# Kernel tuning notes

Hardware: AMD Instinct MI355X
Metric: run time of the kernel (lower is better)

## Reference

```python
import jax, jax.numpy as jnp
import numpy as np

B, N, C = 8, 8192, 91
H = W = 800
SCORE_THRESH = 0.05
NMS_THRESH = 0.5
DET_PER_IMG = 100
BBOX_XFORM_CLIP = float(np.log(1000.0 / 16.0))
WX, WY, WW, WH = 10.0, 10.0, 5.0, 5.0  # bbox_reg_weights


def setup_inputs() -> dict:
    key = jax.random.key(0)
    k1, k2, k3, k4 = jax.random.split(key, 4)
    # realistic xyxy proposals inside the image
    cxcy = jax.random.uniform(k1, (B, N, 2)) * jnp.array([W, H], jnp.float32)
    wh = 8.0 + jax.random.uniform(k2, (B, N, 2)) * 192.0
    x1y1 = jnp.clip(cxcy - 0.5 * wh, 0.0, None)
    x2y2 = jnp.minimum(cxcy + 0.5 * wh, jnp.array([W, H], jnp.float32))
    proposals = jnp.concatenate([x1y1, x2y2], axis=-1)
    class_logits = jax.random.normal(k3, (B, N, C)) * 2.0
    box_regression = jax.random.normal(k4, (B, N, C * 4)) * 0.1
    return {"class_logits": class_logits, "box_regression": box_regression,
            "proposals": proposals}


def _iou_one_many(box, boxes):
    # box [4], boxes [M,4] -> IoU [M] (box_ops.box_iou row)
    lt = jnp.maximum(box[:2], boxes[:, :2])
    rb = jnp.minimum(box[2:], boxes[:, 2:])
    wh = jnp.clip(rb - lt, 0.0, None)
    inter = wh[:, 0] * wh[:, 1]
    a1 = (box[2] - box[0]) * (box[3] - box[1])
    a2 = (boxes[:, 2] - boxes[:, 0]) * (boxes[:, 3] - boxes[:, 1])
    return inter / (a1 + a2 - inter + 1e-9)


def _postprocess_one(logits, codes, props):
    # logits [N,C], codes [N,C,4], props [N,4]
    # --- BoxCoder.decode ---
    widths = props[:, 2] - props[:, 0]
    heights = props[:, 3] - props[:, 1]
    ctr_x = props[:, 0] + 0.5 * widths
    ctr_y = props[:, 1] + 0.5 * heights
    dx = codes[..., 0] / WX
    dy = codes[..., 1] / WY
    dw = jnp.minimum(codes[..., 2] / WW, BBOX_XFORM_CLIP)
    dh = jnp.minimum(codes[..., 3] / WH, BBOX_XFORM_CLIP)
    pcx = dx * widths[:, None] + ctr_x[:, None]
    pcy = dy * heights[:, None] + ctr_y[:, None]
    pw = jnp.exp(dw) * widths[:, None]
    ph = jnp.exp(dh) * heights[:, None]
    boxes = jnp.stack([pcx - 0.5 * pw, pcy - 0.5 * ph,
                       pcx + 0.5 * pw, pcy + 0.5 * ph], axis=-1)  # [N,C,4]
    scores = jax.nn.softmax(logits, axis=-1)
    # --- clip_boxes_to_image ---
    boxes = jnp.stack([jnp.clip(boxes[..., 0], 0.0, float(W)),
                       jnp.clip(boxes[..., 1], 0.0, float(H)),
                       jnp.clip(boxes[..., 2], 0.0, float(W)),
                       jnp.clip(boxes[..., 3], 0.0, float(H))], axis=-1)
    # --- drop background class 0, flatten candidates ---
    boxes = boxes[:, 1:].reshape(-1, 4)          # [M,4], M = N*(C-1)
    scores = scores[:, 1:].reshape(-1)           # [M]
    labels = jnp.tile(jnp.arange(1, C, dtype=jnp.int32), N)  # [M]
    # --- score threshold + remove_small_boxes(min_size=1.0), as masks ---
    ws = boxes[:, 2] - boxes[:, 0]
    hs = boxes[:, 3] - boxes[:, 1]
    valid = (scores > SCORE_THRESH) & (ws >= 1.0) & (hs >= 1.0)
    live = jnp.where(valid, scores, -1.0)
    # --- batched_nms via per-class coordinate offset ---
    off = labels.astype(boxes.dtype) * (float(max(H, W)) + 1.0)
    nboxes = boxes + off[:, None]

    def step(live, _):
        i = jnp.argmax(live)
        s = live[i]
        ious = _iou_one_many(nboxes[i], nboxes)
        live = jnp.where(ious > NMS_THRESH, -1.0, live)
        live = live.at[i].set(-1.0)
        return live, (boxes[i], s, labels[i])

    _, (db, ds, dl) = jax.lax.scan(step, live, None, length=DET_PER_IMG)
    ok = ds > 0.0  # sentinel -1 marks exhausted/invalid slots
    db = jnp.where(ok[:, None], db, 0.0)
    ds = jnp.where(ok, ds, 0.0)
    dl = jnp.where(ok, dl, 0)
    return db, ds, dl, ok


def reference(class_logits, box_regression, proposals):
    codes = box_regression.reshape(B, N, C, 4)
    boxes, scores, labels, valid = jax.vmap(_postprocess_one)(
        class_logits, codes, proposals)
    return boxes, scores, labels, valid
```

## Files before the change

kernel.cpp:

```cpp
#include <hip/hip_runtime.h>

#define BIMG 8
#define NPROP 8192
#define NCLS 91
#define WIMG 800.0f
#define HIMG 800.0f
#define SCORE_T 0.05f
#define NMS_T 0.5f
#define NDET 100
#define CLIPV 4.135166556742356f
#define CNT_STRIDE 16
#define NSURV 100
#define MAXK 512
#define MCACHE 32

__device__ __forceinline__ unsigned long long packkey(float s, int idx) {
    return ((unsigned long long)__float_as_uint(s) << 32) |
           (unsigned long long)(0xFFFFFFFFu - (unsigned int)idx);
}

__global__ void zero_kernel(int* p, int n) {
    int i = blockIdx.x * blockDim.x + threadIdx.x;
    if (i < n) p[i] = 0;
}

__global__ __launch_bounds__(256)
void decode_kernel(const float* __restrict__ logits,
                   const float* __restrict__ creg,
                   const float* __restrict__ props,
                   float* __restrict__ CX1, float* __restrict__ CY1,
                   float* __restrict__ CX2, float* __restrict__ CY2,
                   float* __restrict__ CS, int* __restrict__ CIDX,
                   int* __restrict__ cnt, int capC)
{
    const int wave = blockIdx.x * 4 + (threadIdx.x >> 6);
    const int lane = threadIdx.x & 63;
    const int row = wave;
    const int b = row >> 13;
    const int n = row & (NPROP - 1);

    const float* lrow = logits + (size_t)row * NCLS;
    const float l0 = lrow[lane];
    const float l1 = (lane + 64 < NCLS) ? lrow[lane + 64] : -3.4e38f;

    float m = fmaxf(l0, l1);
    for (int mm = 32; mm > 0; mm >>= 1) m = fmaxf(m, __shfl_xor(m, mm));

    const float e0 = expf(l0 - m);
    const float e1 = (lane + 64 < NCLS) ? expf(l1 - m) : 0.0f;

    float s = e0 + e1;
    for (int mm = 32; mm > 0; mm >>= 1) s += __shfl_xor(s, mm);
    const float denom = __shfl(s, 0);

    const float* p = props + (size_t)row * 4;
    const float px1 = p[0], py1 = p[1], px2 = p[2], py2 = p[3];
    const float w = px2 - px1, h = py2 - py1;
    const float cx = px1 + 0.5f * w, cy = py1 + 0.5f * h;

    for (int half = 0; half < 2; ++half) {
        const int c = lane + half * 64;
        if (c < 1 || c >= NCLS) continue;
        const float score = (half ? e1 : e0) / denom;
        if (!(score > SCORE_T)) continue;

        const float* cd = creg + ((size_t)row * NCLS + c) * 4;
        const float dx = cd[0] / 10.0f;
        const float dy = cd[1] / 10.0f;
        const float dw = fminf(cd[2] / 5.0f, CLIPV);
        const float dh = fminf(cd[3] / 5.0f, CLIPV);
        const float pcx = dx * w + cx, pcy = dy * h + cy;
        const float pw = expf(dw) * w, ph = expf(dh) * h;
        float bx1 = pcx - 0.5f * pw, by1 = pcy - 0.5f * ph;
        float bx2 = pcx + 0.5f * pw, by2 = pcy + 0.5f * ph;
        bx1 = fminf(fmaxf(bx1, 0.0f), WIMG);
        by1 = fminf(fmaxf(by1, 0.0f), HIMG);
        bx2 = fminf(fmaxf(bx2, 0.0f), WIMG);
        by2 = fminf(fmaxf(by2, 0.0f), HIMG);
        if ((bx2 - bx1) >= 1.0f && (by2 - by1) >= 1.0f) {
            const int bc = b * NCLS + c;
            const int k = atomicAdd(&cnt[bc * CNT_STRIDE], 1);
            if (k < capC) {
                const size_t o = (size_t)bc * capC + k;
                CX1[o] = bx1; CY1[o] = by1; CX2[o] = bx2; CY2[o] = by2;
                CS[o] = score;
                CIDX[o] = n * (NCLS - 1) + (c - 1);
            }
        }
    }
}

__global__ __launch_bounds__(256)
void nms_class_kernel(const float* __restrict__ CX1, const float* __restrict__ CY1,
                      const float* __restrict__ CX2, const float* __restrict__ CY2,
                      const float* __restrict__ CS, const int* __restrict__ CIDX,
                      const int* __restrict__ cnt,
                      float* __restrict__ SX1, float* __restrict__ SY1,
                      float* __restrict__ SX2, float* __restrict__ SY2,
                      float* __restrict__ SS, int* __restrict__ SIDX,
                      int* __restrict__ scnt, int capC)
{
    const int bc = blockIdx.x;
    const int c = bc % NCLS;
    const int tid = threadIdx.x;
    const int lane = tid & 63;
    const int wv = tid >> 6;

    int K = 0;
    if (c != 0) {
        K = cnt[bc * CNT_STRIDE];
        if (K > capC) K = capC;
        if (K > MAXK) K = MAXK;
    }
    if (K == 0) { if (tid == 0) scnt[bc] = 0; return; }

    __shared__ float bx1[MAXK], by1[MAXK], bx2[MAXK], by2[MAXK], bs[MAXK];
    __shared__ int bidx[MAXK];
    __shared__ unsigned long long keys[MAXK];
    __shared__ unsigned long long mask[MAXK * 8];
    __shared__ int wseq[NSURV];
    __shared__ int nselsh;

    const size_t base = (size_t)bc * capC;
    for (int i = tid; i < K; i += 256) {
        const float v0 = CX1[base + i], v1 = CY1[base + i];
        const float v2 = CX2[base + i], v3 = CY2[base + i];
        const float sv = CS[base + i];
        const int ix = CIDX[base + i];
        bx1[i] = v0; by1[i] = v1; bx2[i] = v2; by2[i] = v3;
        bs[i] = sv; bidx[i] = ix;
        keys[i] = packkey(sv, ix);
    }
    __syncthreads();

    float* tf = (float*)mask;
    int*   ti = (int*)mask;
    for (int i = tid; i < K; i += 256) {
        const unsigned long long k = keys[i];
        int r = 0;
        for (int j = 0; j < K; ++j) r += (keys[j] > k) ? 1 : 0;
        tf[0 * MAXK + r] = bx1[i];
        tf[1 * MAXK + r] = by1[i];
        tf[2 * MAXK + r] = bx2[i];
        tf[3 * MAXK + r] = by2[i];
        tf[4 * MAXK + r] = bs[i];
        ti[5 * MAXK + r] = bidx[i];
    }
    __syncthreads();
    for (int i = tid; i < K; i += 256) {
        bx1[i] = tf[0 * MAXK + i]; by1[i] = tf[1 * MAXK + i];
        bx2[i] = tf[2 * MAXK + i]; by2[i] = tf[3 * MAXK + i];
        bs[i]  = tf[4 * MAXK + i]; bidx[i] = ti[5 * MAXK + i];
    }
    __syncthreads();

    const float off = (float)c * 801.0f;
    const int W = (K + 63) >> 6;
    for (int w = wv; w < W; w += 4) {
        const int j = (w << 6) + lane;
        const bool jv = (j < K);
        float jx1 = 0, jy1 = 0, jx2 = 0, jy2 = 0;
        if (jv) {
            jx1 = bx1[j] + off; jy1 = by1[j] + off;
            jx2 = bx2[j] + off; jy2 = by2[j] + off;
        }
        const float a2 = (jx2 - jx1) * (jy2 - jy1);
        for (int a = 0; a < K; ++a) {
            const float ax1 = bx1[a] + off, ay1 = by1[a] + off;
            const float ax2 = bx2[a] + off, ay2 = by2[a] + off;
            const float ta = (ax2 - ax1) * (ay2 - ay1);
            bool sup = false;
            if (jv) {
                const float ltx = fmaxf(ax1, jx1), lty = fmaxf(ay1, jy1);
                const float rbx = fminf(ax2, jx2), rby = fminf(ay2, jy2);
                const float iw = fmaxf(rbx - ltx, 0.0f);
                const float ih = fmaxf(rby - lty, 0.0f);
                const float inter = iw * ih;
                const float iou = inter / (ta + a2 - inter + 1e-9f);
                sup = iou > NMS_T;
            }
            const unsigned long long bal = __ballot(sup);
            if (lane == 0) mask[a * 8 + w] = bal;
        }
    }
    __syncthreads();

    if (wv == 0) {
        unsigned long long aw = 0ull;
        if (lane < 8) {
            const int lo = lane << 6;
            if (K > lo) {
                const int nb = K - lo;
                aw = (nb >= 64) ? ~0ull : ((1ull << nb) - 1ull);
            }
        }
        int nsel = 0;
        while (nsel < NSURV) {
            int pos = 0x7fffffff;
            if (aw) pos = (lane << 6) + __builtin_ctzll(aw);
            for (int mm = 32; mm > 0; mm >>= 1)
                pos = min(pos, __shfl_xor(pos, mm));
            if (pos == 0x7fffffff) break;
            if (lane == 0) wseq[nsel] = pos;
            if (lane < 8) aw &= ~mask[(size_t)pos * 8 + lane];
            ++nsel;
        }
        if (lane == 0) nselsh = nsel;
    }
    __syncthreads();

    const int nsel = nselsh;
    for (int t = tid; t < nsel; t += 256) {
        const int a = wseq[t];
        const int sb = bc * NSURV + t;
        SX1[sb] = bx1[a]; SY1[sb] = by1[a];
        SX2[sb] = bx2[a]; SY2[sb] = by2[a];
        SS[sb] = bs[a]; SIDX[sb] = bidx[a];
    }
    if (tid == 0) scnt[bc] = nsel;
}

__global__ __launch_bounds__(256)
void merge_kernel(const float* __restrict__ SX1, const float* __restrict__ SY1,
                  const float* __restrict__ SX2, const float* __restrict__ SY2,
                  const float* __restrict__ SS, const int* __restrict__ SIDX,
                  const int* __restrict__ scnt, float* __restrict__ out)
{
    const int b = blockIdx.x;
    const int tid = threadIdx.x;
    const int lane = tid & 63;
    const int wv = tid >> 6;

    __shared__ unsigned long long kc[NCLS * MCACHE];
    __shared__ int scs[NCLS];
    __shared__ int wseq[NDET];
    __shared__ int stepsh;

    for (int i = tid; i < NCLS; i += 256) scs[i] = scnt[b * NCLS + i];
    __syncthreads();
    for (int t = tid; t < NCLS * MCACHE; t += 256) {
        const int cc = t >> 5, h = t & (MCACHE - 1);
        unsigned long long k = 0ull;
        if (cc >= 1 && h < scs[cc]) {
            const int sb = (b * NCLS + cc) * NSURV + h;
            k = packkey(SS[sb], SIDX[sb]);
        }
        kc[t] = k;
    }
    __syncthreads();

    if (wv == 0) {
        const int c1 = 1 + lane;
        const int c2 = 65 + lane;
        const bool v2 = (c2 < NCLS);
        int h1 = 0, h2 = 0;
        const int s1 = scs[c1];
        const int s2 = v2 ? scs[c2] : 0;
        unsigned long long k1 = (s1 > 0) ? kc[c1 * MCACHE] : 0ull;
        unsigned long long k2 = (s2 > 0) ? kc[c2 * MCACHE] : 0ull;
        int step = 0;
        while (step < NDET) {
            unsigned long long mk = (k1 > k2) ? k1 : k2;
            for (int mm = 32; mm > 0; mm >>= 1) {
                const unsigned long long o = __shfl_xor(mk, mm);
                if (o > mk) mk = o;
            }
            if (mk == 0ull) break;
            if (k1 == mk) {
                wseq[step] = (c1 << 16) | h1;
                ++h1;
                k1 = (h1 < s1)
                     ? (h1 < MCACHE ? kc[c1 * MCACHE + h1]
                                    : packkey(SS[(b * NCLS + c1) * NSURV + h1],
                                              SIDX[(b * NCLS + c1) * NSURV + h1]))
                     : 0ull;
            } else if (k2 == mk) {
                wseq[step] = (c2 << 16) | h2;
                ++h2;
                k2 = (h2 < s2)
                     ? (h2 < MCACHE ? kc[c2 * MCACHE + h2]
                                    : packkey(SS[(b * NCLS + c2) * NSURV + h2],
                                              SIDX[(b * NCLS + c2) * NSURV + h2]))
                     : 0ull;
            }
            ++step;
        }
        if (lane == 0) stepsh = step;
    }
    __syncthreads();

    const int OB = 0, OS = BIMG * NDET * 4, OL = OS + BIMG * NDET,
              OV = OL + BIMG * NDET;
    const int step = stepsh;
    for (int t = tid; t < NDET; t += 256) {
        const int o = b * NDET + t;
        if (t < step) {
            const int cw = wseq[t] >> 16, h = wseq[t] & 0xFFFF;
            const int sb = (b * NCLS + cw) * NSURV + h;
            out[OB + o * 4 + 0] = SX1[sb]; out[OB + o * 4 + 1] = SY1[sb];
            out[OB + o * 4 + 2] = SX2[sb]; out[OB + o * 4 + 3] = SY2[sb];
            out[OS + o] = SS[sb];
            out[OL + o] = (float)cw;
            out[OV + o] = 1.0f;
        } else {
            out[OB + o * 4 + 0] = 0.0f; out[OB + o * 4 + 1] = 0.0f;
            out[OB + o * 4 + 2] = 0.0f; out[OB + o * 4 + 3] = 0.0f;
            out[OS + o] = 0.0f; out[OL + o] = 0.0f; out[OV + o] = 0.0f;
        }
    }
}

extern "C" void kernel_launch(void* const* d_in, const int* in_sizes, int n_in,
                              void* d_out, int out_size, void* d_ws, size_t ws_size,
                              hipStream_t stream) {
    const float* logits = (const float*)d_in[0];
    const float* creg   = (const float*)d_in[1];
    const float* props  = (const float*)d_in[2];
    float* out = (float*)d_out;

    const int nCnt = BIMG * NCLS * CNT_STRIDE;
    const int nZero = nCnt + BIMG * NCLS;
    int* cnt = (int*)d_ws;
    int* scnt = cnt + nCnt;

    const size_t survSlots = (size_t)BIMG * NCLS * NSURV;
    float* SX1 = (float*)((char*)d_ws + 49504);
    float* SY1 = SX1 + survSlots;
    float* SX2 = SY1 + survSlots;
    float* SY2 = SX2 + survSlots;
    float* SS  = SY2 + survSlots;
    int*   SIDX = (int*)(SS + survSlots);

    const size_t clBase = 49504 + survSlots * 6 * 4;
    long capC = 256;
    if (ws_size > clBase) {
        capC = (long)((ws_size - clBase) / ((size_t)BIMG * NCLS * 24));
        capC &= ~63L;
        if (capC < 256) capC = 256;
        if (capC > MAXK) capC = MAXK;
    }
    const size_t clSlots = (size_t)BIMG * NCLS * capC;
    float* CX1 = (float*)((char*)d_ws + clBase);
    float* CY1 = CX1 + clSlots;
    float* CX2 = CY1 + clSlots;
    float* CY2 = CX2 + clSlots;
    float* CS  = CY2 + clSlots;
    int*   CIDX = (int*)(CS + clSlots);

    zero_kernel<<<(nZero + 255) / 256, 256, 0, stream>>>(cnt, nZero);
    decode_kernel<<<BIMG * NPROP / 4, 256, 0, stream>>>(
        logits, creg, props, CX1, CY1, CX2, CY2, CS, CIDX, cnt, (int)capC);
    nms_class_kernel<<<BIMG * NCLS, 256, 0, stream>>>(
        CX1, CY1, CX2, CY2, CS, CIDX, cnt,
        SX1, SY1, SX2, SY2, SS, SIDX, scnt, (int)capC);
    merge_kernel<<<BIMG, 256, 0, stream>>>(
        SX1, SY1, SX2, SY2, SS, SIDX, scnt, out);
}
```

Measured before the change: 492.1 us.

## Pack candidates as float4 boxes plus 64-bit keys, triangular NMS mask, histogram-based top-k merge

Candidate and survivor storage moves from six structure-of-arrays buffers to a float4 box array plus a packed 64-bit score/index key, so loads and stores are vectorized. The IoU mask is now computed only for the upper triangle (j > a), and the greedy NMS selection scans eight words per lane instead of doing a cross-lane shuffle reduction. The serial wave-level k-way merge is replaced by a 1024-thread histogram over score bits, a prefix scan to find the threshold bucket, tie resolution, and rank-by-counting. The histogram bucketing assumes a score range and a MAXTIE cap of 256, which risks wrong results if many keys fall into the threshold bucket.

```diff
diff --git a/kernel.cpp b/kernel.cpp
--- a/kernel.cpp
+++ b/kernel.cpp
@@ -12,11 +12,12 @@
 #define CNT_STRIDE 16
 #define NSURV 100
 #define MAXK 512
-#define MCACHE 32
-
-__device__ __forceinline__ unsigned long long packkey(float s, int idx) {
+#define NBUCK 1024
+#define MAXTIE 256
+
+__device__ __forceinline__ unsigned long long packkey(float s, unsigned int idx) {
     return ((unsigned long long)__float_as_uint(s) << 32) |
-           (unsigned long long)(0xFFFFFFFFu - (unsigned int)idx);
+           (unsigned long long)(0xFFFFFFFFu - idx);
 }
 
 __global__ void zero_kernel(int* p, int n) {
@@ -28,9 +29,8 @@
 void decode_kernel(const float* __restrict__ logits,
                    const float* __restrict__ creg,
                    const float* __restrict__ props,
-                   float* __restrict__ CX1, float* __restrict__ CY1,
-                   float* __restrict__ CX2, float* __restrict__ CY2,
-                   float* __restrict__ CS, int* __restrict__ CIDX,
+                   float4* __restrict__ CBOX,
+                   unsigned long long* __restrict__ CKEY,
                    int* __restrict__ cnt, int capC)
 {
     const int wave = blockIdx.x * 4 + (threadIdx.x >> 6);
@@ -53,10 +53,9 @@
     for (int mm = 32; mm > 0; mm >>= 1) s += __shfl_xor(s, mm);
     const float denom = __shfl(s, 0);
 
-    const float* p = props + (size_t)row * 4;
-    const float px1 = p[0], py1 = p[1], px2 = p[2], py2 = p[3];
-    const float w = px2 - px1, h = py2 - py1;
-    const float cx = px1 + 0.5f * w, cy = py1 + 0.5f * h;
+    const float4 p4 = ((const float4*)props)[row];
+    const float w = p4.z - p4.x, h = p4.w - p4.y;
+    const float cx = p4.x + 0.5f * w, cy = p4.y + 0.5f * h;
 
     for (int half = 0; half < 2; ++half) {
         const int c = lane + half * 64;
@@ -64,11 +63,11 @@
         const float score = (half ? e1 : e0) / denom;
         if (!(score > SCORE_T)) continue;
 
-        const float* cd = creg + ((size_t)row * NCLS + c) * 4;
-        const float dx = cd[0] / 10.0f;
-        const float dy = cd[1] / 10.0f;
-        const float dw = fminf(cd[2] / 5.0f, CLIPV);
-        const float dh = fminf(cd[3] / 5.0f, CLIPV);
+        const float4 cd = ((const float4*)creg)[(size_t)row * NCLS + c];
+        const float dx = cd.x / 10.0f;
+        const float dy = cd.y / 10.0f;
+        const float dw = fminf(cd.z / 5.0f, CLIPV);
+        const float dh = fminf(cd.w / 5.0f, CLIPV);
         const float pcx = dx * w + cx, pcy = dy * h + cy;
         const float pw = expf(dw) * w, ph = expf(dh) * h;
         float bx1 = pcx - 0.5f * pw, by1 = pcy - 0.5f * ph;
@@ -82,22 +81,19 @@
             const int k = atomicAdd(&cnt[bc * CNT_STRIDE], 1);
             if (k < capC) {
                 const size_t o = (size_t)bc * capC + k;
-                CX1[o] = bx1; CY1[o] = by1; CX2[o] = bx2; CY2[o] = by2;
-                CS[o] = score;
-                CIDX[o] = n * (NCLS - 1) + (c - 1);
+                CBOX[o] = make_float4(bx1, by1, bx2, by2);
+                CKEY[o] = packkey(score, (unsigned int)(n * (NCLS - 1) + (c - 1)));
             }
         }
     }
 }
 
 __global__ __launch_bounds__(256)
-void nms_class_kernel(const float* __restrict__ CX1, const float* __restrict__ CY1,
-                      const float* __restrict__ CX2, const float* __restrict__ CY2,
-                      const float* __restrict__ CS, const int* __restrict__ CIDX,
+void nms_class_kernel(const float4* __restrict__ CBOX,
+                      const unsigned long long* __restrict__ CKEY,
                       const int* __restrict__ cnt,
-                      float* __restrict__ SX1, float* __restrict__ SY1,
-                      float* __restrict__ SX2, float* __restrict__ SY2,
-                      float* __restrict__ SS, int* __restrict__ SIDX,
+                      float4* __restrict__ SBOX,
+                      unsigned long long* __restrict__ SKEY,
                       int* __restrict__ scnt, int capC)
 {
     const int bc = blockIdx.x;
@@ -114,44 +110,31 @@
     }
     if (K == 0) { if (tid == 0) scnt[bc] = 0; return; }
 
-    __shared__ float bx1[MAXK], by1[MAXK], bx2[MAXK], by2[MAXK], bs[MAXK];
-    __shared__ int bidx[MAXK];
-    __shared__ unsigned long long keys[MAXK];
-    __shared__ unsigned long long mask[MAXK * 8];
+    __shared__ float4 sbox[MAXK];
+    __shared__ unsigned long long skey[MAXK];
+    __shared__ __align__(16) unsigned long long mask[MAXK * 8];
     __shared__ int wseq[NSURV];
     __shared__ int nselsh;
 
     const size_t base = (size_t)bc * capC;
     for (int i = tid; i < K; i += 256) {
-        const float v0 = CX1[base + i], v1 = CY1[base + i];
-        const float v2 = CX2[base + i], v3 = CY2[base + i];
-        const float sv = CS[base + i];
-        const int ix = CIDX[base + i];
-        bx1[i] = v0; by1[i] = v1; bx2[i] = v2; by2[i] = v3;
-        bs[i] = sv; bidx[i] = ix;
-        keys[i] = packkey(sv, ix);
-    }
-    __syncthreads();
-
-    float* tf = (float*)mask;
-    int*   ti = (int*)mask;
+        sbox[i] = CBOX[base + i];
+        skey[i] = CKEY[base + i];
+    }
+    __syncthreads();
+
+    float4* tb = (float4*)mask;
+    unsigned long long* tk = (unsigned long long*)((char*)mask + MAXK * 16);
     for (int i = tid; i < K; i += 256) {
-        const unsigned long long k = keys[i];
+        const unsigned long long k = skey[i];
         int r = 0;
-        for (int j = 0; j < K; ++j) r += (keys[j] > k) ? 1 : 0;
-        tf[0 * MAXK + r] = bx1[i];
-        tf[1 * MAXK + r] = by1[i];
-        tf[2 * MAXK + r] = bx2[i];
-        tf[3 * MAXK + r] = by2[i];
-        tf[4 * MAXK + r] = bs[i];
-        ti[5 * MAXK + r] = bidx[i];
-    }
-    __syncthreads();
-    for (int i = tid; i < K; i += 256) {
-        bx1[i] = tf[0 * MAXK + i]; by1[i] = tf[1 * MAXK + i];
-        bx2[i] = tf[2 * MAXK + i]; by2[i] = tf[3 * MAXK + i];
-        bs[i]  = tf[4 * MAXK + i]; bidx[i] = ti[5 * MAXK + i];
-    }
+        for (int j = 0; j < K; ++j) r += (skey[j] > k) ? 1 : 0;
+        tb[r] = sbox[i]; tk[r] = k;
+    }
+    __syncthreads();
+    for (int i = tid; i < K; i += 256) { sbox[i] = tb[i]; skey[i] = tk[i]; }
+    __syncthreads();
+    for (int i = tid; i < K * 8; i += 256) mask[i] = 0ull;
     __syncthreads();
 
     const float off = (float)c * 801.0f;
@@ -161,16 +144,19 @@
         const bool jv = (j < K);
         float jx1 = 0, jy1 = 0, jx2 = 0, jy2 = 0;
         if (jv) {
-            jx1 = bx1[j] + off; jy1 = by1[j] + off;
-            jx2 = bx2[j] + off; jy2 = by2[j] + off;
+            const float4 bj = sbox[j];
+            jx1 = bj.x + off; jy1 = bj.y + off;
+            jx2 = bj.z + off; jy2 = bj.w + off;
         }
         const float a2 = (jx2 - jx1) * (jy2 - jy1);
-        for (int a = 0; a < K; ++a) {
-            const float ax1 = bx1[a] + off, ay1 = by1[a] + off;
-            const float ax2 = bx2[a] + off, ay2 = by2[a] + off;
+        const int aend = min(K, (w + 1) << 6);
+        for (int a = 0; a < aend; ++a) {
+            const float4 ba = sbox[a];
+            const float ax1 = ba.x + off, ay1 = ba.y + off;
+            const float ax2 = ba.z + off, ay2 = ba.w + off;
             const float ta = (ax2 - ax1) * (ay2 - ay1);
             bool sup = false;
-            if (jv) {
+            if (jv && j > a) {
                 const float ltx = fmaxf(ax1, jx1), lty = fmaxf(ay1, jy1);
                 const float rbx = fminf(ax2, jx2), rby = fminf(ay2, jy2);
                 const float iw = fmaxf(rbx - ltx, 0.0f);
@@ -186,23 +172,25 @@
     __syncthreads();
 
     if (wv == 0) {
-        unsigned long long aw = 0ull;
-        if (lane < 8) {
-            const int lo = lane << 6;
-            if (K > lo) {
-                const int nb = K - lo;
-                aw = (nb >= 64) ? ~0ull : ((1ull << nb) - 1ull);
-            }
+        unsigned long long aw[8];
+        #pragma unroll
+        for (int w = 0; w < 8; ++w) {
+            const int lo = w << 6;
+            aw[w] = (K > lo) ? ((K - lo >= 64) ? ~0ull : ((1ull << (K - lo)) - 1ull))
+                             : 0ull;
         }
         int nsel = 0;
         while (nsel < NSURV) {
-            int pos = 0x7fffffff;
-            if (aw) pos = (lane << 6) + __builtin_ctzll(aw);
-            for (int mm = 32; mm > 0; mm >>= 1)
-                pos = min(pos, __shfl_xor(pos, mm));
-            if (pos == 0x7fffffff) break;
+            int pos = -1;
+            #pragma unroll
+            for (int w = 0; w < 8; ++w)
+                if (pos < 0 && aw[w]) pos = (w << 6) + __builtin_ctzll(aw[w]);
+            if (pos < 0) break;
             if (lane == 0) wseq[nsel] = pos;
-            if (lane < 8) aw &= ~mask[(size_t)pos * 8 + lane];
+            const unsigned long long* mrow = &mask[(size_t)pos * 8];
+            #pragma unroll
+            for (int w = 0; w < 8; ++w) aw[w] &= ~mrow[w];
+            aw[pos >> 6] &= ~(1ull << (pos & 63));
             ++nsel;
         }
         if (lane == 0) nselsh = nsel;
@@ -212,101 +200,112 @@
     const int nsel = nselsh;
     for (int t = tid; t < nsel; t += 256) {
         const int a = wseq[t];
-        const int sb = bc * NSURV + t;
-        SX1[sb] = bx1[a]; SY1[sb] = by1[a];
-        SX2[sb] = bx2[a]; SY2[sb] = by2[a];
-        SS[sb] = bs[a]; SIDX[sb] = bidx[a];
+        SBOX[bc * NSURV + t] = sbox[a];
+        SKEY[bc * NSURV + t] = skey[a];
     }
     if (tid == 0) scnt[bc] = nsel;
 }
 
-__global__ __launch_bounds__(256)
-void merge_kernel(const float* __restrict__ SX1, const float* __restrict__ SY1,
-                  const float* __restrict__ SX2, const float* __restrict__ SY2,
-                  const float* __restrict__ SS, const int* __restrict__ SIDX,
+__global__ __launch_bounds__(1024)
+void merge_kernel(const float4* __restrict__ SBOX,
+                  const unsigned long long* __restrict__ SKEY,
                   const int* __restrict__ scnt, float* __restrict__ out)
 {
     const int b = blockIdx.x;
     const int tid = threadIdx.x;
-    const int lane = tid & 63;
-    const int wv = tid >> 6;
-
-    __shared__ unsigned long long kc[NCLS * MCACHE];
+
     __shared__ int scs[NCLS];
-    __shared__ int wseq[NDET];
-    __shared__ int stepsh;
-
-    for (int i = tid; i < NCLS; i += 256) scs[i] = scnt[b * NCLS + i];
-    __syncthreads();
-    for (int t = tid; t < NCLS * MCACHE; t += 256) {
-        const int cc = t >> 5, h = t & (MCACHE - 1);
-        unsigned long long k = 0ull;
-        if (cc >= 1 && h < scs[cc]) {
-            const int sb = (b * NCLS + cc) * NSURV + h;
-            k = packkey(SS[sb], SIDX[sb]);
-        }
-        kc[t] = k;
-    }
-    __syncthreads();
-
-    if (wv == 0) {
-        const int c1 = 1 + lane;
-        const int c2 = 65 + lane;
-        const bool v2 = (c2 < NCLS);
-        int h1 = 0, h2 = 0;
-        const int s1 = scs[c1];
-        const int s2 = v2 ? scs[c2] : 0;
-        unsigned long long k1 = (s1 > 0) ? kc[c1 * MCACHE] : 0ull;
-        unsigned long long k2 = (s2 > 0) ? kc[c2 * MCACHE] : 0ull;
-        int step = 0;
-        while (step < NDET) {
-            unsigned long long mk = (k1 > k2) ? k1 : k2;
-            for (int mm = 32; mm > 0; mm >>= 1) {
-                const unsigned long long o = __shfl_xor(mk, mm);
-                if (o > mk) mk = o;
+    __shared__ unsigned int hist[NBUCK];
+    __shared__ unsigned long long selk[NDET];
+    __shared__ int seli[NDET];
+    __shared__ unsigned long long tiek[MAXTIE];
+    __shared__ int tiei[MAXTIE];
+    __shared__ int selc, tiec, Tsh;
+
+    if (tid < NCLS) scs[tid] = scnt[b * NCLS + tid];
+    for (int i = tid; i < NBUCK; i += 1024) hist[i] = 0u;
+    if (tid == 0) { selc = 0; tiec = 0; Tsh = -1; }
+    __syncthreads();
+
+    for (int t = tid; t < NCLS * NSURV; t += 1024) {
+        const int cc = t / NSURV, j = t % NSURV;
+        if (cc >= 1 && j < scs[cc]) {
+            const unsigned long long k = SKEY[(size_t)b * NCLS * NSURV + t];
+            const unsigned int sb32 = (unsigned int)(k >> 32);
+            int bk = (int)((sb32 - 0x3D400000u) >> 16);
+            bk = max(0, min(NBUCK - 1, bk));
+            atomicAdd(&hist[bk], 1u);
+        }
+    }
+    __syncthreads();
+
+    for (int off2 = 1; off2 < NBUCK; off2 <<= 1) {
+        const unsigned int v = (tid + off2 < NBUCK) ? hist[tid + off2] : 0u;
+        __syncthreads();
+        hist[tid] += v;
+        __syncthreads();
+    }
+
+    {
+        const unsigned int g = hist[tid];
+        const unsigned int g1 = (tid + 1 < NBUCK) ? hist[tid + 1] : 0u;
+        if (g > (unsigned)NDET && g1 <= (unsigned)NDET) Tsh = tid;
+    }
+    __syncthreads();
+    const int T = Tsh;
+    const int S = (int)hist[0];
+    const int M = min(NDET, S);
+    const int A = (T + 1 < NBUCK) ? (int)hist[T + 1] : 0;
+    const int need = M - A;
+
+    for (int t = tid; t < NCLS * NSURV; t += 1024) {
+        const int cc = t / NSURV, j = t % NSURV;
+        if (cc >= 1 && j < scs[cc]) {
+            const int sb = b * NCLS * NSURV + t;
+            const unsigned long long k = SKEY[sb];
+            const unsigned int sb32 = (unsigned int)(k >> 32);
+            int bk = (int)((sb32 - 0x3D400000u) >> 16);
+            bk = max(0, min(NBUCK - 1, bk));
+            if (bk > T) {
+                const int p = atomicAdd(&selc, 1);
+                if (p < NDET) { selk[p] = k; seli[p] = sb; }
+            } else if (bk == T) {
+                const int q = atomicAdd(&tiec, 1);
+                if (q < MAXTIE) { tiek[q] = k; tiei[q] = sb; }
             }
-            if (mk == 0ull) break;
-            if (k1 == mk) {
-                wseq[step] = (c1 << 16) | h1;
-                ++h1;
-                k1 = (h1 < s1)
-                     ? (h1 < MCACHE ? kc[c1 * MCACHE + h1]
-                                    : packkey(SS[(b * NCLS + c1) * NSURV + h1],
-                                              SIDX[(b * NCLS + c1) * NSURV + h1]))
-                     : 0ull;
-            } else if (k2 == mk) {
-                wseq[step] = (c2 << 16) | h2;
-                ++h2;
-                k2 = (h2 < s2)
-                     ? (h2 < MCACHE ? kc[c2 * MCACHE + h2]
-                                    : packkey(SS[(b * NCLS + c2) * NSURV + h2],
-                                              SIDX[(b * NCLS + c2) * NSURV + h2]))
-                     : 0ull;
-            }
-            ++step;
-        }
-        if (lane == 0) stepsh = step;
+        }
+    }
+    __syncthreads();
+
+    const int nt = min(tiec, MAXTIE);
+    for (int q = tid; q < nt; q += 1024) {
+        const unsigned long long k = tiek[q];
+        int r = 0;
+        for (int j2 = 0; j2 < nt; ++j2) r += (tiek[j2] > k) ? 1 : 0;
+        if (r < need) { selk[A + r] = k; seli[A + r] = tiei[q]; }
     }
     __syncthreads();
 
     const int OB = 0, OS = BIMG * NDET * 4, OL = OS + BIMG * NDET,
               OV = OL + BIMG * NDET;
-    const int step = stepsh;
-    for (int t = tid; t < NDET; t += 256) {
-        const int o = b * NDET + t;
-        if (t < step) {
-            const int cw = wseq[t] >> 16, h = wseq[t] & 0xFFFF;
-            const int sb = (b * NCLS + cw) * NSURV + h;
-            out[OB + o * 4 + 0] = SX1[sb]; out[OB + o * 4 + 1] = SY1[sb];
-            out[OB + o * 4 + 2] = SX2[sb]; out[OB + o * 4 + 3] = SY2[sb];
-            out[OS + o] = SS[sb];
-            out[OL + o] = (float)cw;
-            out[OV + o] = 1.0f;
-        } else {
-            out[OB + o * 4 + 0] = 0.0f; out[OB + o * 4 + 1] = 0.0f;
-            out[OB + o * 4 + 2] = 0.0f; out[OB + o * 4 + 3] = 0.0f;
-            out[OS + o] = 0.0f; out[OL + o] = 0.0f; out[OV + o] = 0.0f;
-        }
+    for (int mi = tid; mi < M; mi += 1024) {
+        const unsigned long long k = selk[mi];
+        int r = 0;
+        for (int j2 = 0; j2 < M; ++j2) r += (selk[j2] > k) ? 1 : 0;
+        const float4 bx = SBOX[seli[mi]];
+        const int o = b * NDET + r;
+        out[OB + o * 4 + 0] = bx.x; out[OB + o * 4 + 1] = bx.y;
+        out[OB + o * 4 + 2] = bx.z; out[OB + o * 4 + 3] = bx.w;
+        const unsigned int idx = 0xFFFFFFFFu - (unsigned int)k;
+        out[OS + o] = __uint_as_float((unsigned int)(k >> 32));
+        out[OL + o] = (float)((int)(idx % (NCLS - 1)) + 1);
+        out[OV + o] = 1.0f;
+    }
+    for (int mi = M + tid; mi < NDET; mi += 1024) {
+        const int o = b * NDET + mi;
+        out[OB + o * 4 + 0] = 0.0f; out[OB + o * 4 + 1] = 0.0f;
+        out[OB + o * 4 + 2] = 0.0f; out[OB + o * 4 + 3] = 0.0f;
+        out[OS + o] = 0.0f; out[OL + o] = 0.0f; out[OV + o] = 0.0f;
     }
 }
 
@@ -324,14 +323,10 @@
     int* scnt = cnt + nCnt;
 
     const size_t survSlots = (size_t)BIMG * NCLS * NSURV;
-    float* SX1 = (float*)((char*)d_ws + 49504);
-    float* SY1 = SX1 + survSlots;
-    float* SX2 = SY1 + survSlots;
-    float* SY2 = SX2 + survSlots;
-    float* SS  = SY2 + survSlots;
-    int*   SIDX = (int*)(SS + survSlots);
-
-    const size_t clBase = 49504 + survSlots * 6 * 4;
+    float4* SBOX = (float4*)((char*)d_ws + 49504);
+    unsigned long long* SKEY = (unsigned long long*)(SBOX + survSlots);
+
+    const size_t clBase = 49504 + survSlots * 24;
     long capC = 256;
     if (ws_size > clBase) {
         capC = (long)((ws_size - clBase) / ((size_t)BIMG * NCLS * 24));
@@ -340,19 +335,13 @@
         if (capC > MAXK) capC = MAXK;
     }
     const size_t clSlots = (size_t)BIMG * NCLS * capC;
-    float* CX1 = (float*)((char*)d_ws + clBase);
-    float* CY1 = CX1 + clSlots;
-    float* CX2 = CY1 + clSlots;
-    float* CY2 = CX2 + clSlots;
-    float* CS  = CY2 + clSlots;
-    int*   CIDX = (int*)(CS + clSlots);
+    float4* CBOX = (float4*)((char*)d_ws + clBase);
+    unsigned long long* CKEY = (unsigned long long*)(CBOX + clSlots);
 
     zero_kernel<<<(nZero + 255) / 256, 256, 0, stream>>>(cnt, nZero);
     decode_kernel<<<BIMG * NPROP / 4, 256, 0, stream>>>(
-        logits, creg, props, CX1, CY1, CX2, CY2, CS, CIDX, cnt, (int)capC);
+        logits, creg, props, CBOX, CKEY, cnt, (int)capC);
     nms_class_kernel<<<BIMG * NCLS, 256, 0, stream>>>(
-        CX1, CY1, CX2, CY2, CS, CIDX, cnt,
-        SX1, SY1, SX2, SY2, SS, SIDX, scnt, (int)capC);
-    merge_kernel<<<BIMG, 256, 0, stream>>>(
-        SX1, SY1, SX2, SY2, SS, SIDX, scnt, out);
-}
+        CBOX, CKEY, cnt, SBOX, SKEY, scnt, (int)capC);
+    merge_kernel<<<BIMG, 1024, 0, stream>>>(SBOX, SKEY, scnt, out);
+}
```

Measured after the change: 406.3 us. 17.4% less time.
